# Kernel optimization log

Measured on AMD Instinct MI355X. Metric: run time of the kernel, lower is better.

The kernel has to match this reference:

```python
import jax, jax.numpy as jnp
import numpy as np

BN_EPS = 1e-5


def setup_inputs() -> dict:
    key = jax.random.key(0)
    k_x, k_w, k_g, k_b, k_m, k_v = jax.random.split(key, 6)
    B, P, C = 8, 512, 1024
    x = jax.random.normal(k_x, (B, P, C), dtype=jnp.float32)
    # Linear(dim, dim, bias=False) weight, torch layout (out, in)
    W_qkv = jax.random.normal(k_w, (C, C), dtype=jnp.float32) * (1.0 / np.sqrt(C))
    # BatchNorm1d(dim) eval-mode params over channel axis
    bn_gamma = jnp.ones((C,), jnp.float32) + 0.01 * jax.random.normal(k_g, (C,), dtype=jnp.float32)
    bn_beta = 0.01 * jax.random.normal(k_b, (C,), dtype=jnp.float32)
    bn_mean = 0.01 * jax.random.normal(k_m, (C,), dtype=jnp.float32)
    bn_var = jnp.abs(1.0 + 0.01 * jax.random.normal(k_v, (C,), dtype=jnp.float32))
    gra_sharp = jnp.float32(2.0)
    return {"x": x, "W_qkv": W_qkv, "bn_gamma": bn_gamma, "bn_beta": bn_beta,
            "bn_mean": bn_mean, "bn_var": bn_var, "gra_sharp": gra_sharp}


def reference(x, W_qkv, bn_gamma, bn_beta, bn_mean, bn_var, gra_sharp):
    B, P, C = x.shape
    H = 8  # num_heads
    Wd = P // H  # per-head token width (heads split the SEQUENCE axis)

    # shared Linear(dim,dim,bias=False); q = k = v since same module on same x
    qkv = jnp.einsum('bpc,dc->bpd', x, W_qkv)          # (B, P, C)
    qkv = qkv.transpose(0, 2, 1)                        # (B, C, P)
    # BatchNorm1d(dim), eval mode: normalize channel axis (dim=1)
    inv = jax.lax.rsqrt(bn_var + BN_EPS)
    qkv = (qkv - bn_mean[None, :, None]) * (inv * bn_gamma)[None, :, None] + bn_beta[None, :, None]

    # split_last((H, -1)) on seq axis then transpose(1,2): (B, H, C, Wd)
    q = qkv.reshape(B, C, H, Wd).transpose(0, 2, 1, 3)
    k = q
    v = q

    # channel-by-channel scores per head: (B, H, C, C)
    scores = jnp.einsum('bhcw,bhdw->bhcd', q, k) / gra_sharp
    # NON-STANDARD: softmax over the HEAD axis (dim=1); dropout = identity (eval)
    attn = jax.nn.softmax(scores, axis=1)

    h = jnp.einsum('bhcd,bhdw->bhcw', attn, v)          # (B, H, C, Wd)
    h = h.transpose(0, 2, 1, 3).reshape(B, C, P)        # merge heads back into P
    h = h.transpose(0, 2, 1)                            # (B, P, C)
    return h, attn
```

## Files before the change

kernel.cpp:

```cpp
#include <hip/hip_runtime.h>
#include <math.h>

#define B 8
#define P 512
#define C 1024
#define H 8
#define BN_EPS 1e-5f

typedef __attribute__((ext_vector_type(8))) __bf16 bf16x8;
typedef __attribute__((ext_vector_type(4))) __bf16 bf16x4;
typedef __attribute__((ext_vector_type(4))) float f32x4;

__global__ __launch_bounds__(256) void split_hi_lo(
    const float* __restrict__ x, const float* __restrict__ Wq,
    __bf16* __restrict__ xhi, __bf16* __restrict__ xlo,
    __bf16* __restrict__ whi, __bf16* __restrict__ wlo)
{
    const size_t NX4 = (size_t)B * P * C / 4;
    size_t idx = (size_t)blockIdx.x * 256 + threadIdx.x;
    float4 v;
    __bf16 *dh, *dl;
    size_t o;
    if (idx < NX4) {
        v = ((const float4*)x)[idx];
        dh = xhi; dl = xlo; o = idx * 4;
    } else {
        v = ((const float4*)Wq)[idx - NX4];
        dh = whi; dl = wlo; o = (idx - NX4) * 4;
    }
    float f[4] = {v.x, v.y, v.z, v.w};
    bf16x4 hv, lv;
    #pragma unroll
    for (int j = 0; j < 4; ++j) {
        __bf16 hb = (__bf16)f[j];
        hv[j] = hb;
        lv[j] = (__bf16)(f[j] - (float)hb);
    }
    *(bf16x4*)&dh[o] = hv;
    *(bf16x4*)&dl[o] = lv;
}

__global__ __launch_bounds__(256) void qkv_bn_mfma(
    const __bf16* __restrict__ xhi, const __bf16* __restrict__ xlo,
    const __bf16* __restrict__ whi, const __bf16* __restrict__ wlo,
    const float* __restrict__ gamma, const float* __restrict__ beta,
    const float* __restrict__ mean, const float* __restrict__ var,
    __bf16* __restrict__ Yhi, __bf16* __restrict__ Ylo, __bf16* __restrict__ Zhi)
{
    const int dt = blockIdx.x;
    const int pt = blockIdx.y;
    const int b  = blockIdx.z;
    const int t = threadIdx.x, lane = t & 63, wid = t >> 6;
    const int quadd = (wid >> 1) * 32, quadp = (wid & 1) * 32;
    const int lr = lane & 15, lk = (lane >> 4) * 8;

    const int drow0 = dt * 64 + quadd + lr;
    const size_t xrow0 = ((size_t)b * P + pt * 64 + quadp + lr) * C;

    f32x4 acc[2][2];
    #pragma unroll
    for (int tm = 0; tm < 2; ++tm)
        #pragma unroll
        for (int tn = 0; tn < 2; ++tn)
            acc[tm][tn] = (f32x4){0.f, 0.f, 0.f, 0.f};

    for (int c0 = 0; c0 < C; c0 += 32) {
        const int col = c0 + lk;
        bf16x8 ah[2], al[2], bh[2], bl[2];
        #pragma unroll
        for (int tm = 0; tm < 2; ++tm) {
            size_t ia = (size_t)(drow0 + tm * 16) * C + col;
            ah[tm] = *(const bf16x8*)&whi[ia];
            al[tm] = *(const bf16x8*)&wlo[ia];
        }
        #pragma unroll
        for (int tn = 0; tn < 2; ++tn) {
            size_t ib = xrow0 + (size_t)tn * 16 * C + col;
            bh[tn] = *(const bf16x8*)&xhi[ib];
            bl[tn] = *(const bf16x8*)&xlo[ib];
        }
        #pragma unroll
        for (int tm = 0; tm < 2; ++tm)
            #pragma unroll
            for (int tn = 0; tn < 2; ++tn) {
                acc[tm][tn] = __builtin_amdgcn_mfma_f32_16x16x32_bf16(ah[tm], bh[tn], acc[tm][tn], 0, 0, 0);
                acc[tm][tn] = __builtin_amdgcn_mfma_f32_16x16x32_bf16(ah[tm], bl[tn], acc[tm][tn], 0, 0, 0);
                acc[tm][tn] = __builtin_amdgcn_mfma_f32_16x16x32_bf16(al[tm], bh[tn], acc[tm][tn], 0, 0, 0);
            }
    }

    const int rgrp = (lane >> 4) * 4;
    #pragma unroll
    for (int tm = 0; tm < 2; ++tm) {
        const int dbase = dt * 64 + quadd + tm * 16 + rgrp;
        float4 g4 = *(const float4*)&gamma[dbase];
        float4 bb4 = *(const float4*)&beta[dbase];
        float4 m4 = *(const float4*)&mean[dbase];
        float4 v4 = *(const float4*)&var[dbase];
        float gf[4] = {g4.x, g4.y, g4.z, g4.w};
        float bf[4] = {bb4.x, bb4.y, bb4.z, bb4.w};
        float mf[4] = {m4.x, m4.y, m4.z, m4.w};
        float vf[4] = {v4.x, v4.y, v4.z, v4.w};
        float sc[4];
        #pragma unroll
        for (int r = 0; r < 4; ++r) sc[r] = rsqrtf(vf[r] + BN_EPS) * gf[r];

        #pragma unroll
        for (int tn = 0; tn < 2; ++tn) {
            const int p = pt * 64 + quadp + tn * 16 + lr;
            bf16x4 zq;
            #pragma unroll
            for (int r = 0; r < 4; ++r) {
                float n = (acc[tm][tn][r] - mf[r]) * sc[r] + bf[r];
                __bf16 hb = (__bf16)n;
                __bf16 lb = (__bf16)(n - (float)hb);
                size_t yi = ((size_t)b * C + dbase + r) * P + p;
                Yhi[yi] = hb;
                Ylo[yi] = lb;
                zq[r] = hb;
            }
            *(bf16x4*)&Zhi[((size_t)b * P + p) * C + dbase] = zq;
        }
    }
}

__global__ __launch_bounds__(256, 2) void attn_fused(
    const __bf16* __restrict__ Yhi, const __bf16* __restrict__ Ylo,
    const __bf16* __restrict__ Zhi, const float* __restrict__ gs_ptr,
    float* __restrict__ attn, float* __restrict__ out0)
{
    const int id = blockIdx.x;
    const int b  = id & 7;
    const int ct = id >> 3;
    const int c0 = ct * 16;
    const int t = threadIdx.x, lane = t & 63, w = t >> 6;
    const int lr = lane & 15, lk = (lane >> 4) * 8, rgrp = (lane >> 4) * 4;
    const float scale = 1.0f / gs_ptr[0];

    __shared__ __bf16 Plds[8][16][72];
    __shared__ float Olds[64][20];

    const size_t YbaseC = ((size_t)b * C + c0 + lr) * P;
    bf16x8 ah[16];
    #pragma unroll
    for (int h = 0; h < H; ++h)
        #pragma unroll
        for (int s = 0; s < 2; ++s)
            ah[h * 2 + s] = *(const bf16x8*)&Yhi[YbaseC + h * 64 + s * 32 + lk];

    f32x4 out_acc[8];
    #pragma unroll
    for (int h = 0; h < H; ++h) out_acc[h] = (f32x4){0.f, 0.f, 0.f, 0.f};

    for (int dbase = 0; dbase < C; dbase += 64) {
        const int drow = dbase + w * 16 + lr;
        const size_t YbaseD = ((size_t)b * C + drow) * P;

        f32x4 sacc[8];
        #pragma unroll
        for (int h = 0; h < H; ++h) sacc[h] = (f32x4){0.f, 0.f, 0.f, 0.f};

        #pragma unroll
        for (int h = 0; h < H; ++h) {
            #pragma unroll
            for (int s = 0; s < 2; ++s) {
                const int col = h * 64 + s * 32 + lk;
                bf16x8 bh = *(const bf16x8*)&Yhi[YbaseD + col];
                bf16x8 bl = *(const bf16x8*)&Ylo[YbaseD + col];
                bf16x8 av = *(const bf16x8*)&Ylo[YbaseC + col];
                sacc[h] = __builtin_amdgcn_mfma_f32_16x16x32_bf16(ah[h * 2 + s], bh, sacc[h], 0, 0, 0);
                sacc[h] = __builtin_amdgcn_mfma_f32_16x16x32_bf16(ah[h * 2 + s], bl, sacc[h], 0, 0, 0);
                sacc[h] = __builtin_amdgcn_mfma_f32_16x16x32_bf16(av, bh, sacc[h], 0, 0, 0);
            }
        }

        const int dcol = dbase + w * 16 + lr;
        #pragma unroll
        for (int r = 0; r < 4; ++r) {
            const int c = c0 + rgrp + r;
            float v[8];
            float m = -1e30f;
            #pragma unroll
            for (int h = 0; h < H; ++h) {
                v[h] = sacc[h][r] * scale;
                m = fmaxf(m, v[h]);
            }
            float ssum = 0.f;
            #pragma unroll
            for (int h = 0; h < H; ++h) { v[h] = __expf(v[h] - m); ssum += v[h]; }
            float inv = 1.0f / ssum;
            #pragma unroll
            for (int h = 0; h < H; ++h) {
                float p = v[h] * inv;
                attn[(((size_t)(b * H + h) * C + c) * C) + dcol] = p;
                Plds[h][rgrp + r][w * 16 + lr] = (__bf16)p;
            }
        }

        bf16x8 bv[8][2];
        #pragma unroll
        for (int h = 0; h < H; ++h) {
            const int p = h * 64 + w * 16 + lr;
            #pragma unroll
            for (int kh = 0; kh < 2; ++kh)
                bv[h][kh] = *(const bf16x8*)&Zhi[((size_t)b * P + p) * C + dbase + kh * 32 + lk];
        }
        __syncthreads();

        #pragma unroll
        for (int h = 0; h < H; ++h) {
            #pragma unroll
            for (int kh = 0; kh < 2; ++kh) {
                bf16x8 a = *(const bf16x8*)&Plds[h][lr][kh * 32 + lk];
                out_acc[h] = __builtin_amdgcn_mfma_f32_16x16x32_bf16(a, bv[h][kh], out_acc[h], 0, 0, 0);
            }
        }
        __syncthreads();
    }

    #pragma unroll
    for (int h = 0; h < H; ++h) {
        #pragma unroll
        for (int r = 0; r < 4; ++r)
            Olds[w * 16 + lr][rgrp + r] = out_acc[h][r];
        __syncthreads();
        {
            const int row = t >> 2;
            const int coff = (t & 3) * 4;
            f32x4 vv = *(const f32x4*)&Olds[row][coff];
            *(f32x4*)&out0[((size_t)b * P + h * 64 + row) * C + c0 + coff] = vv;
        }
        __syncthreads();
    }
}

extern "C" void kernel_launch(void* const* d_in, const int* in_sizes, int n_in,
                              void* d_out, int out_size, void* d_ws, size_t ws_size,
                              hipStream_t stream) {
    const float* x     = (const float*)d_in[0];
    const float* Wq    = (const float*)d_in[1];
    const float* gamma = (const float*)d_in[2];
    const float* beta  = (const float*)d_in[3];
    const float* mean  = (const float*)d_in[4];
    const float* var   = (const float*)d_in[5];
    const float* gs    = (const float*)d_in[6];

    float* out0 = (float*)d_out;
    float* attn = (float*)d_out + (size_t)B * P * C;

    const size_t NE = (size_t)B * C * P;
    __bf16* Yhi = (__bf16*)d_ws;
    __bf16* Ylo = Yhi + NE;
    __bf16* Zhi = Ylo + NE;

    const size_t attn_elems = (size_t)B * H * C * C;
    __bf16* S = (__bf16*)(attn + (attn_elems - 5242880));
    __bf16* xhi = S;
    __bf16* xlo = xhi + (size_t)B * P * C;
    __bf16* whi = xlo + (size_t)B * P * C;
    __bf16* wlo = whi + (size_t)C * C;

    split_hi_lo<<<5120, 256, 0, stream>>>(x, Wq, xhi, xlo, whi, wlo);
    qkv_bn_mfma<<<dim3(16, 8, 8), 256, 0, stream>>>(xhi, xlo, whi, wlo,
                                                    gamma, beta, mean, var,
                                                    Yhi, Ylo, Zhi);
    attn_fused<<<512, 256, 0, stream>>>(Yhi, Ylo, Zhi, gs, attn, out0);
}
```

Before: 331.9 us.

## Split d-range across waves with per-wave accumulation and cross-wave reduction

```diff
diff --git a/kernel.cpp b/kernel.cpp
--- a/kernel.cpp
+++ b/kernel.cpp
@@ -134,27 +134,27 @@
     const int ct = id >> 3;
     const int c0 = ct * 16;
     const int t = threadIdx.x, lane = t & 63, w = t >> 6;
-    const int lr = lane & 15, lk = (lane >> 4) * 8, rgrp = (lane >> 4) * 4;
+    const int lc = lane & 15;
+    const int lg = lane >> 4;
+    const int lk = lg * 8;
+    const int rgrp = lg * 4;
     const float scale = 1.0f / gs_ptr[0];
 
-    __shared__ __bf16 Plds[8][16][72];
-    __shared__ float Olds[64][20];
-
-    const size_t YbaseC = ((size_t)b * C + c0 + lr) * P;
-    bf16x8 ah[16];
+    __shared__ __align__(16) float  Tbuf[4][16][20];
+    __shared__ __align__(16) __bf16 Pbuf[4][8][16][40];
+
+    f32x4 out_acc[8][4];
     #pragma unroll
     for (int h = 0; h < H; ++h)
         #pragma unroll
-        for (int s = 0; s < 2; ++s)
-            ah[h * 2 + s] = *(const bf16x8*)&Yhi[YbaseC + h * 64 + s * 32 + lk];
-
-    f32x4 out_acc[8];
-    #pragma unroll
-    for (int h = 0; h < H; ++h) out_acc[h] = (f32x4){0.f, 0.f, 0.f, 0.f};
-
-    for (int dbase = 0; dbase < C; dbase += 64) {
-        const int drow = dbase + w * 16 + lr;
-        const size_t YbaseD = ((size_t)b * C + drow) * P;
+        for (int pt = 0; pt < 4; ++pt)
+            out_acc[h][pt] = (f32x4){0.f, 0.f, 0.f, 0.f};
+
+    const size_t cbase = ((size_t)b * C + c0 + lc) * P;
+
+    for (int it = 0; it < 16; ++it) {
+        const int dwin = w * 256 + it * 16;
+        const size_t dbase = ((size_t)b * C + dwin + lc) * P;
 
         f32x4 sacc[8];
         #pragma unroll
@@ -165,19 +165,18 @@
             #pragma unroll
             for (int s = 0; s < 2; ++s) {
                 const int col = h * 64 + s * 32 + lk;
-                bf16x8 bh = *(const bf16x8*)&Yhi[YbaseD + col];
-                bf16x8 bl = *(const bf16x8*)&Ylo[YbaseD + col];
-                bf16x8 av = *(const bf16x8*)&Ylo[YbaseC + col];
-                sacc[h] = __builtin_amdgcn_mfma_f32_16x16x32_bf16(ah[h * 2 + s], bh, sacc[h], 0, 0, 0);
-                sacc[h] = __builtin_amdgcn_mfma_f32_16x16x32_bf16(ah[h * 2 + s], bl, sacc[h], 0, 0, 0);
-                sacc[h] = __builtin_amdgcn_mfma_f32_16x16x32_bf16(av, bh, sacc[h], 0, 0, 0);
-            }
-        }
-
-        const int dcol = dbase + w * 16 + lr;
+                bf16x8 dh_ = *(const bf16x8*)&Yhi[dbase + col];
+                bf16x8 dl_ = *(const bf16x8*)&Ylo[dbase + col];
+                bf16x8 ch_ = *(const bf16x8*)&Yhi[cbase + col];
+                bf16x8 cl_ = *(const bf16x8*)&Ylo[cbase + col];
+                sacc[h] = __builtin_amdgcn_mfma_f32_16x16x32_bf16(dh_, ch_, sacc[h], 0, 0, 0);
+                sacc[h] = __builtin_amdgcn_mfma_f32_16x16x32_bf16(dh_, cl_, sacc[h], 0, 0, 0);
+                sacc[h] = __builtin_amdgcn_mfma_f32_16x16x32_bf16(dl_, ch_, sacc[h], 0, 0, 0);
+            }
+        }
+
         #pragma unroll
         for (int r = 0; r < 4; ++r) {
-            const int c = c0 + rgrp + r;
             float v[8];
             float m = -1e30f;
             #pragma unroll
@@ -190,46 +189,51 @@
             for (int h = 0; h < H; ++h) { v[h] = __expf(v[h] - m); ssum += v[h]; }
             float inv = 1.0f / ssum;
             #pragma unroll
+            for (int h = 0; h < H; ++h) sacc[h][r] = v[h] * inv;
+        }
+
+        const int half = it & 1;
+        const int cpr = lane >> 2;
+        const int dpr = (lane & 3) * 4;
+        #pragma unroll
+        for (int h = 0; h < H; ++h) {
+            *(f32x4*)&Tbuf[w][lc][rgrp] = sacc[h];
+            bf16x4 pq;
+            #pragma unroll
+            for (int r = 0; r < 4; ++r) pq[r] = (__bf16)sacc[h][r];
+            *(bf16x4*)&Pbuf[w][h][lc][half * 16 + rgrp] = pq;
+            f32x4 av_ = *(const f32x4*)&Tbuf[w][cpr][dpr];
+            *(f32x4*)&attn[(((size_t)(b * H + h) * C) + c0 + cpr) * C + dwin + dpr] = av_;
+        }
+
+        if (half == 1) {
+            const int d2 = w * 256 + (it - 1) * 16;
+            #pragma unroll
             for (int h = 0; h < H; ++h) {
-                float p = v[h] * inv;
-                attn[(((size_t)(b * H + h) * C + c) * C) + dcol] = p;
-                Plds[h][rgrp + r][w * 16 + lr] = (__bf16)p;
-            }
-        }
-
-        bf16x8 bv[8][2];
-        #pragma unroll
-        for (int h = 0; h < H; ++h) {
-            const int p = h * 64 + w * 16 + lr;
-            #pragma unroll
-            for (int kh = 0; kh < 2; ++kh)
-                bv[h][kh] = *(const bf16x8*)&Zhi[((size_t)b * P + p) * C + dbase + kh * 32 + lk];
-        }
+                bf16x8 pb = *(const bf16x8*)&Pbuf[w][h][lc][lk];
+                #pragma unroll
+                for (int pt = 0; pt < 4; ++pt) {
+                    bf16x8 av = *(const bf16x8*)&Zhi[((size_t)b * P + h * 64 + pt * 16 + lc) * C + d2 + lk];
+                    out_acc[h][pt] = __builtin_amdgcn_mfma_f32_16x16x32_bf16(av, pb, out_acc[h][pt], 0, 0, 0);
+                }
+            }
+        }
+    }
+
+    __syncthreads();
+    float* cb = (float*)&Pbuf[0][0][0][0];
+    for (int h = 0; h < H; ++h) {
+        #pragma unroll
+        for (int pt = 0; pt < 4; ++pt)
+            *(f32x4*)&cb[(((w * 4) + pt) * 64 + lane) * 4] = out_acc[h][pt];
         __syncthreads();
-
-        #pragma unroll
-        for (int h = 0; h < H; ++h) {
-            #pragma unroll
-            for (int kh = 0; kh < 2; ++kh) {
-                bf16x8 a = *(const bf16x8*)&Plds[h][lr][kh * 32 + lk];
-                out_acc[h] = __builtin_amdgcn_mfma_f32_16x16x32_bf16(a, bv[h][kh], out_acc[h], 0, 0, 0);
-            }
-        }
-        __syncthreads();
-    }
-
-    #pragma unroll
-    for (int h = 0; h < H; ++h) {
+        f32x4 s = (f32x4){0.f, 0.f, 0.f, 0.f};
+        #pragma unroll
+        for (int w2 = 0; w2 < 4; ++w2)
+            s += *(const f32x4*)&cb[((w2 * 4 + w) * 64 + lane) * 4];
         #pragma unroll
         for (int r = 0; r < 4; ++r)
-            Olds[w * 16 + lr][rgrp + r] = out_acc[h][r];
-        __syncthreads();
-        {
-            const int row = t >> 2;
-            const int coff = (t & 3) * 4;
-            f32x4 vv = *(const f32x4*)&Olds[row][coff];
-            *(f32x4*)&out0[((size_t)b * P + h * 64 + row) * C + c0 + coff] = vv;
-        }
+            out0[((size_t)b * P + h * 64 + w * 16 + rgrp + r) * C + c0 + lc] = s[r];
         __syncthreads();
     }
 }
```

Result: slower. 433.8 us (+30.7%).

## Split attention reduction over d into two halves with atomic accumulation

Applied to the files above, without the earlier changes.

```diff
diff --git a/kernel.cpp b/kernel.cpp
--- a/kernel.cpp
+++ b/kernel.cpp
@@ -40,6 +40,12 @@
     *(bf16x4*)&dl[o] = lv;
 }
 
+__global__ __launch_bounds__(256) void zero_out0(float* __restrict__ out0)
+{
+    size_t i = ((size_t)blockIdx.x * 256 + threadIdx.x) * 4;
+    *(f32x4*)&out0[i] = (f32x4){0.f, 0.f, 0.f, 0.f};
+}
+
 __global__ __launch_bounds__(256) void qkv_bn_mfma(
     const __bf16* __restrict__ xhi, const __bf16* __restrict__ xlo,
     const __bf16* __restrict__ whi, const __bf16* __restrict__ wlo,
@@ -124,37 +130,36 @@
     }
 }
 
-__global__ __launch_bounds__(256, 2) void attn_fused(
+__global__ __launch_bounds__(256, 4) void attn_fused(
     const __bf16* __restrict__ Yhi, const __bf16* __restrict__ Ylo,
     const __bf16* __restrict__ Zhi, const float* __restrict__ gs_ptr,
     float* __restrict__ attn, float* __restrict__ out0)
 {
     const int id = blockIdx.x;
     const int b  = id & 7;
-    const int ct = id >> 3;
+    const int ct = (id >> 3) & 63;
+    const int dh = id >> 9;
     const int c0 = ct * 16;
     const int t = threadIdx.x, lane = t & 63, w = t >> 6;
-    const int lr = lane & 15, lk = (lane >> 4) * 8, rgrp = (lane >> 4) * 4;
+    const int lr = lane & 15;
+    const int lg = lane >> 4;
+    const int lk = lg * 8;
+    const int rgrp = lg * 4;
     const float scale = 1.0f / gs_ptr[0];
 
     __shared__ __bf16 Plds[8][16][72];
     __shared__ float Olds[64][20];
 
-    const size_t YbaseC = ((size_t)b * C + c0 + lr) * P;
-    bf16x8 ah[16];
-    #pragma unroll
-    for (int h = 0; h < H; ++h)
-        #pragma unroll
-        for (int s = 0; s < 2; ++s)
-            ah[h * 2 + s] = *(const bf16x8*)&Yhi[YbaseC + h * 64 + s * 32 + lk];
-
     f32x4 out_acc[8];
     #pragma unroll
     for (int h = 0; h < H; ++h) out_acc[h] = (f32x4){0.f, 0.f, 0.f, 0.f};
 
-    for (int dbase = 0; dbase < C; dbase += 64) {
-        const int drow = dbase + w * 16 + lr;
-        const size_t YbaseD = ((size_t)b * C + drow) * P;
+    const size_t cbase = ((size_t)b * C + c0 + lr) * P;
+
+    for (int it = 0; it < 8; ++it) {
+        const int dwin0 = dh * 512 + it * 64;
+        const int dwin  = dwin0 + w * 16;
+        const size_t dbase = ((size_t)b * C + dwin + lr) * P;
 
         f32x4 sacc[8];
         #pragma unroll
@@ -165,16 +170,17 @@
             #pragma unroll
             for (int s = 0; s < 2; ++s) {
                 const int col = h * 64 + s * 32 + lk;
-                bf16x8 bh = *(const bf16x8*)&Yhi[YbaseD + col];
-                bf16x8 bl = *(const bf16x8*)&Ylo[YbaseD + col];
-                bf16x8 av = *(const bf16x8*)&Ylo[YbaseC + col];
-                sacc[h] = __builtin_amdgcn_mfma_f32_16x16x32_bf16(ah[h * 2 + s], bh, sacc[h], 0, 0, 0);
-                sacc[h] = __builtin_amdgcn_mfma_f32_16x16x32_bf16(ah[h * 2 + s], bl, sacc[h], 0, 0, 0);
-                sacc[h] = __builtin_amdgcn_mfma_f32_16x16x32_bf16(av, bh, sacc[h], 0, 0, 0);
-            }
-        }
-
-        const int dcol = dbase + w * 16 + lr;
+                bf16x8 ch_ = *(const bf16x8*)&Yhi[cbase + col];
+                bf16x8 cl_ = *(const bf16x8*)&Ylo[cbase + col];
+                bf16x8 bh_ = *(const bf16x8*)&Yhi[dbase + col];
+                bf16x8 bl_ = *(const bf16x8*)&Ylo[dbase + col];
+                sacc[h] = __builtin_amdgcn_mfma_f32_16x16x32_bf16(ch_, bh_, sacc[h], 0, 0, 0);
+                sacc[h] = __builtin_amdgcn_mfma_f32_16x16x32_bf16(ch_, bl_, sacc[h], 0, 0, 0);
+                sacc[h] = __builtin_amdgcn_mfma_f32_16x16x32_bf16(cl_, bh_, sacc[h], 0, 0, 0);
+            }
+        }
+
+        const int dcol = dwin + lr;
         #pragma unroll
         for (int r = 0; r < 4; ++r) {
             const int c = c0 + rgrp + r;
@@ -196,23 +202,16 @@
                 Plds[h][rgrp + r][w * 16 + lr] = (__bf16)p;
             }
         }
-
-        bf16x8 bv[8][2];
+        __syncthreads();
+
         #pragma unroll
         for (int h = 0; h < H; ++h) {
             const int p = h * 64 + w * 16 + lr;
             #pragma unroll
-            for (int kh = 0; kh < 2; ++kh)
-                bv[h][kh] = *(const bf16x8*)&Zhi[((size_t)b * P + p) * C + dbase + kh * 32 + lk];
-        }
-        __syncthreads();
-
-        #pragma unroll
-        for (int h = 0; h < H; ++h) {
-            #pragma unroll
             for (int kh = 0; kh < 2; ++kh) {
+                bf16x8 bv = *(const bf16x8*)&Zhi[((size_t)b * P + p) * C + dwin0 + kh * 32 + lk];
                 bf16x8 a = *(const bf16x8*)&Plds[h][lr][kh * 32 + lk];
-                out_acc[h] = __builtin_amdgcn_mfma_f32_16x16x32_bf16(a, bv[h][kh], out_acc[h], 0, 0, 0);
+                out_acc[h] = __builtin_amdgcn_mfma_f32_16x16x32_bf16(a, bv, out_acc[h], 0, 0, 0);
             }
         }
         __syncthreads();
@@ -228,7 +227,9 @@
             const int row = t >> 2;
             const int coff = (t & 3) * 4;
             f32x4 vv = *(const f32x4*)&Olds[row][coff];
-            *(f32x4*)&out0[((size_t)b * P + h * 64 + row) * C + c0 + coff] = vv;
+            float* dst = &out0[((size_t)b * P + h * 64 + row) * C + c0 + coff];
+            #pragma unroll
+            for (int j = 0; j < 4; ++j) unsafeAtomicAdd(dst + j, vv[j]);
         }
         __syncthreads();
     }
@@ -261,8 +262,9 @@
     __bf16* wlo = whi + (size_t)C * C;
 
     split_hi_lo<<<5120, 256, 0, stream>>>(x, Wq, xhi, xlo, whi, wlo);
+    zero_out0<<<4096, 256, 0, stream>>>(out0);
     qkv_bn_mfma<<<dim3(16, 8, 8), 256, 0, stream>>>(xhi, xlo, whi, wlo,
                                                     gamma, beta, mean, var,
                                                     Yhi, Ylo, Zhi);
-    attn_fused<<<512, 256, 0, stream>>>(Yhi, Ylo, Zhi, gs, attn, out0);
-}
+    attn_fused<<<1024, 256, 0, stream>>>(Yhi, Ylo, Zhi, gs, attn, out0);
+}
```

Measured after the change: 539.8 us. 1.63x slower.
